# Kernel optimization log

Hardware: AMD Instinct MI355X
Metric: run time of the kernel (lower is better)

## Reference

```python
import jax, jax.numpy as jnp
import numpy as np

QMIN = 0.0
QMAX = 255.0  # uint8, asymmetric


def fake_quant(x, scale, zp):
    # asymmetric uint8 fake-quantization: q = clamp(round(x/s + zp), 0, 255); dq = (q - zp) * s
    s = scale.reshape(())
    z = zp.reshape(())
    q = jnp.clip(jnp.round(x / s + z), QMIN, QMAX)
    return (q - z) * s


def setup_inputs() -> dict:
    key = jax.random.key(0)
    k1, k2 = jax.random.split(key)
    B, M, K, N = 4, 2048, 4096, 4096
    x1 = jax.random.normal(k1, (B, M, K), dtype=jnp.float32)
    x2 = jax.random.normal(k2, (B, K, N), dtype=jnp.float32)
    # realistic learned per-tensor scale / zero-point for ~N(0,1) data over uint8 range
    x1_scale = jnp.full((1,), 8.0 / 255.0, dtype=jnp.float32)
    x1_zp = jnp.full((1,), 128.0, dtype=jnp.float32)
    x2_scale = jnp.full((1,), 8.0 / 255.0, dtype=jnp.float32)
    x2_zp = jnp.full((1,), 128.0, dtype=jnp.float32)
    return {"x1": x1, "x2": x2, "x1_scale": x1_scale, "x1_zp": x1_zp,
            "x2_scale": x2_scale, "x2_zp": x2_zp}


def reference(x1, x2, x1_scale, x1_zp, x2_scale, x2_zp):
    q1 = fake_quant(x1, x1_scale, x1_zp)  # [B, M, K]
    q2 = fake_quant(x2, x2_scale, x2_zp)  # [B, K, N]
    return jnp.matmul(q1, q2)             # [B, M, N]
```

## Files before the change

kernel.cpp:

```cpp
#include <hip/hip_runtime.h>
#include <stdint.h>

typedef int v4i __attribute__((ext_vector_type(4)));

#define GLOBAL_AS __attribute__((address_space(1)))
#define LDS_AS __attribute__((address_space(3)))

__device__ __forceinline__ int quant1(float x, float s, float z, int zi) {
    float q = rintf(x / s + z);
    q = fminf(fmaxf(q, 0.0f), 255.0f);
    return (int)q - zi;
}

__device__ __forceinline__ unsigned qpack4(float4 v, float s, float z, int zi) {
    unsigned q0 = (unsigned)(quant1(v.x, s, z, zi) & 255);
    unsigned q1 = (unsigned)(quant1(v.y, s, z, zi) & 255);
    unsigned q2 = (unsigned)(quant1(v.z, s, z, zi) & 255);
    unsigned q3 = (unsigned)(quant1(v.w, s, z, zi) & 255);
    return q0 | (q1 << 8) | (q2 << 16) | (q3 << 24);
}

__global__ __launch_bounds__(256) void quant_lin(const float* __restrict__ x,
                                                 int8_t* __restrict__ out,
                                                 const float* __restrict__ sp,
                                                 const float* __restrict__ zp,
                                                 long n16) {
    float s = sp[0], z = zp[0];
    int zi = (int)rintf(z);
    long i = (long)blockIdx.x * 256 + threadIdx.x;
    if (i >= n16) return;
    const float4* xv = (const float4*)x;
    uint4 w;
    w.x = qpack4(xv[i * 4 + 0], s, z, zi);
    w.y = qpack4(xv[i * 4 + 1], s, z, zi);
    w.z = qpack4(xv[i * 4 + 2], s, z, zi);
    w.w = qpack4(xv[i * 4 + 3], s, z, zi);
    ((uint4*)out)[i] = w;
}

__global__ __launch_bounds__(256) void quant_bt(const float* __restrict__ x,
                                                int8_t* __restrict__ out,
                                                const float* __restrict__ sp,
                                                const float* __restrict__ zp) {
    constexpr int K = 4096, N = 4096;
    float s = sp[0], z = zp[0];
    int zi = (int)rintf(z);
    size_t bin = (size_t)blockIdx.z * K * N;
    int tid = threadIdx.x;
    int bk = tid >> 4;
    int bn = tid & 15;
    int k0 = blockIdx.y * 64, n0 = blockIdx.x * 64;
    __shared__ unsigned lds[64][17];
    unsigned o0 = 0, o1 = 0, o2 = 0, o3 = 0;
#pragma unroll
    for (int r = 0; r < 4; ++r) {
        float4 v = *(const float4*)(x + bin + (size_t)(k0 + bk * 4 + r) * N + n0 + bn * 4);
        o0 |= (unsigned)(quant1(v.x, s, z, zi) & 255) << (r * 8);
        o1 |= (unsigned)(quant1(v.y, s, z, zi) & 255) << (r * 8);
        o2 |= (unsigned)(quant1(v.z, s, z, zi) & 255) << (r * 8);
        o3 |= (unsigned)(quant1(v.w, s, z, zi) & 255) << (r * 8);
    }
    lds[bn * 4 + 0][bk] = o0;
    lds[bn * 4 + 1][bk] = o1;
    lds[bn * 4 + 2][bk] = o2;
    lds[bn * 4 + 3][bk] = o3;
    __syncthreads();
    int nl = tid >> 2, ch = tid & 3;
    uint4 w;
    w.x = lds[nl][ch * 4 + 0];
    w.y = lds[nl][ch * 4 + 1];
    w.z = lds[nl][ch * 4 + 2];
    w.w = lds[nl][ch * 4 + 3];
    *(uint4*)(out + bin + (size_t)(n0 + nl) * K + k0 + ch * 16) = w;
}

__global__ __launch_bounds__(256, 2) void gemm_i8(const int8_t* __restrict__ A,
                                                  const int8_t* __restrict__ Bt,
                                                  float* __restrict__ C,
                                                  const float* __restrict__ sp1,
                                                  const float* __restrict__ sp2) {
    constexpr int M = 2048, N = 4096, K = 4096;
    constexpr int BM = 256, BN = 128, BK = 64;
    constexpr int NT = K / BK;
    constexpr int NBN = N / BN;
    constexpr int SLOT = 24576;

    extern __shared__ char smem[];

    int b = blockIdx.z;
    const int8_t* Ab = A + (size_t)b * M * K;
    const int8_t* Bb = Bt + (size_t)b * N * K;
    float* Cb = C + (size_t)b * M * N;

    int nwg = gridDim.x;
    int wg = blockIdx.x;
    wg = (wg & 7) * (nwg >> 3) + (wg >> 3);
    int by = wg / NBN, bx = wg % NBN;
    int m0 = by * BM, n0 = bx * BN;

    int tid = threadIdx.x;
    int lane = tid & 63, wid = tid >> 6;
    int wr = wid >> 1, wc = wid & 1;
    int l15 = lane & 15, cb = lane >> 4;

    int row0 = tid >> 2, cc0 = tid & 3;
    int sw0 = cc0 ^ ((row0 >> 1) & 3);
    const size_t JSTEP = (size_t)64 * K;
    const int8_t* pAi = Ab + (size_t)(m0 + row0) * K + sw0 * 16;
    const int8_t* pBi = Bb + (size_t)(n0 + row0) * K + sw0 * 16;
    const unsigned dbase = (unsigned)tid * 16;

    int aoff[8], boff[4];
#pragma unroll
    for (int m = 0; m < 8; ++m) {
        int r = wr * 128 + m * 16 + l15;
        aoff[m] = r * 64 + ((cb ^ ((r >> 1) & 3)) * 16);
    }
#pragma unroll
    for (int n = 0; n < 4; ++n) {
        int r = wc * 64 + n * 16 + l15;
        boff[n] = 16384 + r * 64 + ((cb ^ ((r >> 1) & 3)) * 16);
    }

    v4i zero = {0, 0, 0, 0};
    v4i acc[8][4];
#pragma unroll
    for (int m = 0; m < 8; ++m)
#pragma unroll
        for (int n = 0; n < 4; ++n) acc[m][n] = zero;

#define ISSUE(S)                                                                       \
    {                                                                                  \
        char* da = smem + (S)*SLOT + dbase;                                            \
        _Pragma("unroll") for (int j = 0; j < 4; ++j)                                  \
            __builtin_amdgcn_global_load_lds((const GLOBAL_AS void*)(pAi + j * JSTEP), \
                                             (LDS_AS void*)(da + j * 4096), 16, 0, 0); \
        char* db = smem + (S)*SLOT + 16384 + dbase;                                    \
        _Pragma("unroll") for (int j = 0; j < 2; ++j)                                  \
            __builtin_amdgcn_global_load_lds((const GLOBAL_AS void*)(pBi + j * JSTEP), \
                                             (LDS_AS void*)(db + j * 4096), 16, 0, 0); \
        pAi += BK;                                                                     \
        pBi += BK;                                                                     \
    }

#define TILE(S, DOISSUE, DOWAIT)                                                       \
    {                                                                                  \
        const char* Ar = smem + (S)*SLOT;                                              \
        v4i af[8], bf[4];                                                              \
        _Pragma("unroll") for (int n = 0; n < 4; ++n)                                  \
            bf[n] = *(const v4i*)(Ar + boff[n]);                                       \
        _Pragma("unroll") for (int m = 0; m < 8; ++m)                                  \
            af[m] = *(const v4i*)(Ar + aoff[m]);                                       \
        DOISSUE;                                                                       \
        __builtin_amdgcn_s_setprio(1);                                                 \
        _Pragma("unroll") for (int m = 0; m < 8; ++m)                                  \
            _Pragma("unroll") for (int n = 0; n < 4; ++n)                              \
                acc[m][n] = __builtin_amdgcn_mfma_i32_16x16x64_i8(af[m], bf[n],        \
                                                                  acc[m][n], 0, 0, 0); \
        __builtin_amdgcn_s_setprio(0);                                                 \
        DOWAIT;                                                                        \
    }

#define W6                                                                             \
    asm volatile("s_waitcnt lgkmcnt(0)\n\ts_waitcnt vmcnt(6)" ::: "memory");           \
    __builtin_amdgcn_s_barrier();                                                      \
    asm volatile("" ::: "memory");
#define W0                                                                             \
    asm volatile("s_waitcnt lgkmcnt(0)\n\ts_waitcnt vmcnt(0)" ::: "memory");           \
    __builtin_amdgcn_s_barrier();                                                      \
    asm volatile("" ::: "memory");

    ISSUE(0);
    ISSUE(1);
    asm volatile("s_waitcnt vmcnt(6)" ::: "memory");
    __builtin_amdgcn_s_barrier();
    asm volatile("" ::: "memory");

    for (int tt = 0; tt < 60; tt += 3) {
        TILE(0, ISSUE(2), W6)
        TILE(1, ISSUE(0), W6)
        TILE(2, ISSUE(1), W6)
    }
    TILE(0, ISSUE(2), W6)
    TILE(1, ISSUE(0), W6)
    TILE(2, , W0)
    TILE(0, , )

    float sc = sp1[0] * sp2[0];
    int r0 = cb * 4;
#pragma unroll
    for (int m = 0; m < 8; ++m) {
#pragma unroll
        for (int n = 0; n < 4; ++n) {
            float* p = Cb + (size_t)(m0 + wr * 128 + m * 16 + r0) * N +
                       (n0 + wc * 64 + n * 16 + l15);
#pragma unroll
            for (int r = 0; r < 4; ++r) p[(size_t)r * N] = sc * (float)acc[m][n][r];
        }
    }
#undef ISSUE
#undef TILE
#undef W6
#undef W0
}

extern "C" void kernel_launch(void* const* d_in, const int* in_sizes, int n_in,
                              void* d_out, int out_size, void* d_ws, size_t ws_size,
                              hipStream_t stream) {
    const float* x1 = (const float*)d_in[0];
    const float* x2 = (const float*)d_in[1];
    const float* s1 = (const float*)d_in[2];
    const float* z1 = (const float*)d_in[3];
    const float* s2 = (const float*)d_in[4];
    const float* z2 = (const float*)d_in[5];
    float* out = (float*)d_out;

    const int B = 4, M = 2048, K = 4096, N = 4096;
    const size_t ASZ = (size_t)B * M * K;
    const size_t BSZ = (size_t)B * K * N;
    dim3 blk(256);

    static int lds_attr_set = 0;
    if (!lds_attr_set) {
        (void)hipFuncSetAttribute((const void*)gemm_i8,
                                  hipFuncAttributeMaxDynamicSharedMemorySize, 73728);
        lds_attr_set = 1;
    }

    if (ws_size >= ASZ + BSZ) {
        int8_t* Aq = (int8_t*)d_ws;
        int8_t* Bq = Aq + ASZ;
        long n16 = (long)(ASZ / 16);
        quant_lin<<<dim3((unsigned)(n16 / 256)), blk, 0, stream>>>(x1, Aq, s1, z1, n16);
        quant_bt<<<dim3(N / 64, K / 64, B), blk, 0, stream>>>(x2, Bq, s2, z2);
        gemm_i8<<<dim3((M / 256) * (N / 128), 1, B), dim3(256), 73728, stream>>>(
            Aq, Bq, out, s1, s2);
    } else {
        const size_t AB = (size_t)M * K, BB = (size_t)K * N;
        int8_t* Aq = (int8_t*)d_ws;
        int8_t* Bq = Aq + AB;
        for (int b = 0; b < B; ++b) {
            long n16 = (long)(AB / 16);
            quant_lin<<<dim3((unsigned)(n16 / 256)), blk, 0, stream>>>(x1 + (size_t)b * AB, Aq, s1, z1, n16);
            quant_bt<<<dim3(N / 64, K / 64, 1), blk, 0, stream>>>(x2 + (size_t)b * BB, Bq, s2, z2);
            gemm_i8<<<dim3((M / 256) * (N / 128), 1, 1), dim3(256), 73728, stream>>>(
                Aq, Bq, out + (size_t)b * M * N, s1, s2);
        }
    }
}
```

Measured before the change: 262.4 us.

## Enlarge GEMM tile to 256x256 with 4-stage LDS ring and register double-buffering

Raises the int8 GEMM block tile from 256x128 to 256x256, giving each wave 8x8 MFMA accumulators, and drops occupancy to one workgroup per CU. The pipeline changes from a 3-slot LDS ring to a 4-slot ring of 32KB slots. Fragments are double-buffered in registers, so LDS reads for the next tile overlap MFMAs on the current one. This aims to raise arithmetic intensity and hide LDS latency, at the cost of heavy VGPR/AGPR pressure (256 accumulator registers plus fragments), possible spills, and fewer workgroups (512 vs 1024) for latency hiding.

```diff
diff --git a/kernel.cpp b/kernel.cpp
--- a/kernel.cpp
+++ b/kernel.cpp
@@ -74,16 +74,14 @@
     *(uint4*)(out + bin + (size_t)(n0 + nl) * K + k0 + ch * 16) = w;
 }
 
-__global__ __launch_bounds__(256, 2) void gemm_i8(const int8_t* __restrict__ A,
+__global__ __launch_bounds__(256, 1) void gemm_i8(const int8_t* __restrict__ A,
                                                   const int8_t* __restrict__ Bt,
                                                   float* __restrict__ C,
                                                   const float* __restrict__ sp1,
                                                   const float* __restrict__ sp2) {
     constexpr int M = 2048, N = 4096, K = 4096;
-    constexpr int BM = 256, BN = 128, BK = 64;
-    constexpr int NT = K / BK;
+    constexpr int BM = 256, BN = 256;
     constexpr int NBN = N / BN;
-    constexpr int SLOT = 24576;
 
     extern __shared__ char smem[];
 
@@ -103,105 +101,104 @@
     int wr = wid >> 1, wc = wid & 1;
     int l15 = lane & 15, cb = lane >> 4;
 
-    int row0 = tid >> 2, cc0 = tid & 3;
-    int sw0 = cc0 ^ ((row0 >> 1) & 3);
-    const size_t JSTEP = (size_t)64 * K;
-    const int8_t* pAi = Ab + (size_t)(m0 + row0) * K + sw0 * 16;
-    const int8_t* pBi = Bb + (size_t)(n0 + row0) * K + sw0 * 16;
+    const int8_t* Abase = Ab + (size_t)m0 * K;
+    const int8_t* Bbase = Bb + (size_t)n0 * K;
+
+    int r0 = tid >> 2, cc0 = tid & 3;
+    int sw0 = cc0 ^ ((r0 >> 1) & 3);
+    const size_t JR = (size_t)64 * K;
+    const int8_t* pA = Abase + (size_t)r0 * K + sw0 * 16;
+    const int8_t* pB = Bbase + (size_t)r0 * K + sw0 * 16;
     const unsigned dbase = (unsigned)tid * 16;
 
-    int aoff[8], boff[4];
+    int aoff[8], boff[8];
 #pragma unroll
     for (int m = 0; m < 8; ++m) {
         int r = wr * 128 + m * 16 + l15;
         aoff[m] = r * 64 + ((cb ^ ((r >> 1) & 3)) * 16);
     }
 #pragma unroll
-    for (int n = 0; n < 4; ++n) {
-        int r = wc * 64 + n * 16 + l15;
+    for (int n = 0; n < 8; ++n) {
+        int r = wc * 128 + n * 16 + l15;
         boff[n] = 16384 + r * 64 + ((cb ^ ((r >> 1) & 3)) * 16);
     }
 
     v4i zero = {0, 0, 0, 0};
-    v4i acc[8][4];
+    v4i acc[8][8];
 #pragma unroll
     for (int m = 0; m < 8; ++m)
 #pragma unroll
-        for (int n = 0; n < 4; ++n) acc[m][n] = zero;
-
-#define ISSUE(S)                                                                       \
-    {                                                                                  \
-        char* da = smem + (S)*SLOT + dbase;                                            \
-        _Pragma("unroll") for (int j = 0; j < 4; ++j)                                  \
-            __builtin_amdgcn_global_load_lds((const GLOBAL_AS void*)(pAi + j * JSTEP), \
-                                             (LDS_AS void*)(da + j * 4096), 16, 0, 0); \
-        char* db = smem + (S)*SLOT + 16384 + dbase;                                    \
-        _Pragma("unroll") for (int j = 0; j < 2; ++j)                                  \
-            __builtin_amdgcn_global_load_lds((const GLOBAL_AS void*)(pBi + j * JSTEP), \
-                                             (LDS_AS void*)(db + j * 4096), 16, 0, 0); \
-        pAi += BK;                                                                     \
-        pBi += BK;                                                                     \
-    }
-
-#define TILE(S, DOISSUE, DOWAIT)                                                       \
-    {                                                                                  \
-        const char* Ar = smem + (S)*SLOT;                                              \
-        v4i af[8], bf[4];                                                              \
-        _Pragma("unroll") for (int n = 0; n < 4; ++n)                                  \
-            bf[n] = *(const v4i*)(Ar + boff[n]);                                       \
-        _Pragma("unroll") for (int m = 0; m < 8; ++m)                                  \
-            af[m] = *(const v4i*)(Ar + aoff[m]);                                       \
-        DOISSUE;                                                                       \
-        __builtin_amdgcn_s_setprio(1);                                                 \
-        _Pragma("unroll") for (int m = 0; m < 8; ++m)                                  \
-            _Pragma("unroll") for (int n = 0; n < 4; ++n)                              \
-                acc[m][n] = __builtin_amdgcn_mfma_i32_16x16x64_i8(af[m], bf[n],        \
-                                                                  acc[m][n], 0, 0, 0); \
-        __builtin_amdgcn_s_setprio(0);                                                 \
-        DOWAIT;                                                                        \
-    }
-
-#define W6                                                                             \
-    asm volatile("s_waitcnt lgkmcnt(0)\n\ts_waitcnt vmcnt(6)" ::: "memory");           \
-    __builtin_amdgcn_s_barrier();                                                      \
-    asm volatile("" ::: "memory");
-#define W0                                                                             \
-    asm volatile("s_waitcnt lgkmcnt(0)\n\ts_waitcnt vmcnt(0)" ::: "memory");           \
-    __builtin_amdgcn_s_barrier();                                                      \
+        for (int n = 0; n < 8; ++n) acc[m][n] = zero;
+
+    v4i a0[8], b0[8], a1[8], b1[8];
+
+#define ISSUE(S)                                                                        \
+    {                                                                                   \
+        char* da = smem + (S)*32768 + dbase;                                            \
+        _Pragma("unroll") for (int j = 0; j < 4; ++j)                                   \
+            __builtin_amdgcn_global_load_lds((const GLOBAL_AS void*)(pA + j * JR),      \
+                                             (LDS_AS void*)(da + j * 4096), 16, 0, 0);  \
+        char* db = smem + (S)*32768 + 16384 + dbase;                                    \
+        _Pragma("unroll") for (int j = 0; j < 4; ++j)                                   \
+            __builtin_amdgcn_global_load_lds((const GLOBAL_AS void*)(pB + j * JR),      \
+                                             (LDS_AS void*)(db + j * 4096), 16, 0, 0);  \
+        pA += 64;                                                                       \
+        pB += 64;                                                                       \
+    }
+
+#define RD(S, fa, fb)                                                                   \
+    {                                                                                   \
+        const char* rb = smem + (S)*32768;                                              \
+        _Pragma("unroll") for (int n = 0; n < 8; ++n)                                   \
+            fb[n] = *(const v4i*)(rb + boff[n]);                                        \
+        _Pragma("unroll") for (int m = 0; m < 8; ++m)                                   \
+            fa[m] = *(const v4i*)(rb + aoff[m]);                                        \
+    }
+
+#define MM(fa, fb)                                                                      \
+    _Pragma("unroll") for (int m = 0; m < 8; ++m)                                       \
+        _Pragma("unroll") for (int n = 0; n < 8; ++n)                                   \
+            acc[m][n] = __builtin_amdgcn_mfma_i32_16x16x64_i8(fa[m], fb[n],             \
+                                                              acc[m][n], 0, 0, 0);
+
+#define WAITBAR(NW)                                                                     \
+    asm volatile("s_waitcnt vmcnt(" #NW ")" ::: "memory");                              \
+    __builtin_amdgcn_s_barrier();                                                       \
     asm volatile("" ::: "memory");
 
     ISSUE(0);
     ISSUE(1);
-    asm volatile("s_waitcnt vmcnt(6)" ::: "memory");
-    __builtin_amdgcn_s_barrier();
-    asm volatile("" ::: "memory");
-
-    for (int tt = 0; tt < 60; tt += 3) {
-        TILE(0, ISSUE(2), W6)
-        TILE(1, ISSUE(0), W6)
-        TILE(2, ISSUE(1), W6)
-    }
-    TILE(0, ISSUE(2), W6)
-    TILE(1, ISSUE(0), W6)
-    TILE(2, , W0)
-    TILE(0, , )
+    ISSUE(2);
+    WAITBAR(8)
+    RD(0, a0, b0);
+
+    for (int it = 0; it < 15; ++it) {
+        ISSUE(3); RD(1, a1, b1); MM(a0, b0) WAITBAR(8)
+        ISSUE(0); RD(2, a0, b0); MM(a1, b1) WAITBAR(8)
+        ISSUE(1); RD(3, a1, b1); MM(a0, b0) WAITBAR(8)
+        ISSUE(2); RD(0, a0, b0); MM(a1, b1) WAITBAR(8)
+    }
+    ISSUE(3); RD(1, a1, b1); MM(a0, b0) WAITBAR(8)
+    RD(2, a0, b0); MM(a1, b1) WAITBAR(0)
+    RD(3, a1, b1); MM(a0, b0)
+    MM(a1, b1)
 
     float sc = sp1[0] * sp2[0];
-    int r0 = cb * 4;
+    int rr = cb * 4;
 #pragma unroll
     for (int m = 0; m < 8; ++m) {
 #pragma unroll
-        for (int n = 0; n < 4; ++n) {
-            float* p = Cb + (size_t)(m0 + wr * 128 + m * 16 + r0) * N +
-                       (n0 + wc * 64 + n * 16 + l15);
+        for (int n = 0; n < 8; ++n) {
+            float* p = Cb + (size_t)(m0 + wr * 128 + m * 16 + rr) * N +
+                       (n0 + wc * 128 + n * 16 + l15);
 #pragma unroll
             for (int r = 0; r < 4; ++r) p[(size_t)r * N] = sc * (float)acc[m][n][r];
         }
     }
 #undef ISSUE
-#undef TILE
-#undef W6
-#undef W0
+#undef RD
+#undef MM
+#undef WAITBAR
 }
 
 extern "C" void kernel_launch(void* const* d_in, const int* in_sizes, int n_in,
@@ -223,7 +220,7 @@
     static int lds_attr_set = 0;
     if (!lds_attr_set) {
         (void)hipFuncSetAttribute((const void*)gemm_i8,
-                                  hipFuncAttributeMaxDynamicSharedMemorySize, 73728);
+                                  hipFuncAttributeMaxDynamicSharedMemorySize, 131072);
         lds_attr_set = 1;
     }
 
@@ -233,7 +230,7 @@
         long n16 = (long)(ASZ / 16);
         quant_lin<<<dim3((unsigned)(n16 / 256)), blk, 0, stream>>>(x1, Aq, s1, z1, n16);
         quant_bt<<<dim3(N / 64, K / 64, B), blk, 0, stream>>>(x2, Bq, s2, z2);
-        gemm_i8<<<dim3((M / 256) * (N / 128), 1, B), dim3(256), 73728, stream>>>(
+        gemm_i8<<<dim3((M / 256) * (N / 256), 1, B), dim3(256), 131072, stream>>>(
             Aq, Bq, out, s1, s2);
     } else {
         const size_t AB = (size_t)M * K, BB = (size_t)K * N;
@@ -243,7 +240,7 @@
             long n16 = (long)(AB / 16);
             quant_lin<<<dim3((unsigned)(n16 / 256)), blk, 0, stream>>>(x1 + (size_t)b * AB, Aq, s1, z1, n16);
             quant_bt<<<dim3(N / 64, K / 64, 1), blk, 0, stream>>>(x2 + (size_t)b * BB, Bq, s2, z2);
-            gemm_i8<<<dim3((M / 256) * (N / 128), 1, 1), dim3(256), 73728, stream>>>(
+            gemm_i8<<<dim3((M / 256) * (N / 256), 1, 1), dim3(256), 131072, stream>>>(
                 Aq, Bq, out + (size_t)b * M * N, s1, s2);
         }
     }
```

New measurement: 269.6 us. 1.03x slower.
